# Performance work log

Measured on AMD Instinct MI355X. Metric: run time of the kernel, lower is better.

## Reference

```python
import jax, jax.numpy as jnp
import numpy as np

N = 6
DT = 0.02
EPS = 1e-6
_R, _C = np.tril_indices(N)  # row-major lower-triangle order, matches the torch double loop


def _mlp(x, W1, b1, W2, b2, W3, b3):
    h = jax.nn.softplus(x @ W1 + b1)
    h = jax.nn.softplus(h @ W2 + b2)
    return h @ W3 + b3


def _trig(q):
    # interleaved [cos q0, sin q0, cos q1, sin q1, ...]
    return jnp.stack([jnp.cos(q), jnp.sin(q)], axis=-1).reshape(q.shape[:-1] + (2 * N,))


def _mass_single(q, pL):
    # q: (6,) -> M: (6,6)
    y = _mlp(_trig(q), *pL)  # (21,)
    L = jnp.zeros((N, N), y.dtype).at[_R, _C].set(y)
    return L @ L.T + EPS * jnp.eye(N, dtype=y.dtype)


def _mass_batched(q, pL):
    y = _mlp(_trig(q), *pL)  # (B,21)
    L = jnp.zeros((q.shape[0], N, N), y.dtype).at[:, _R, _C].set(y)
    return jnp.einsum('bik,bjk->bij', L, L) + EPS * jnp.eye(N, dtype=y.dtype)


def _pot_batched(q, pV):
    return _mlp(_trig(q), *pV)[:, 0]  # (B,)


def _get_acc(q, qdot, a, pL, pV):
    M = _mass_batched(q, pL)                                   # (B,6,6)
    # per-sample Jacobian dM[i,j]/dq[k] -> (B,6,6,6)
    dM_dq = jax.vmap(jax.jacfwd(lambda qq: _mass_single(qq, pL)))(q)
    # torch: term_1[b,i,j,l] = sum_k M[b,l,k] * dM[b,j,k]/dq[b,i]
    term1 = jnp.einsum('blk,bjki->bijl', M, dM_dq)
    dM = term1 + term1.swapaxes(2, 3)
    c = (jnp.einsum('bjik,bk,bj->bi', dM, qdot, qdot)
         - 0.5 * jnp.einsum('bikj,bk,bj->bi', dM, qdot, qdot))
    # faithful to torch.cholesky_inverse(M): inverse of tril(M) @ tril(M)^T
    Linv = jnp.linalg.inv(jnp.tril(M))
    Minv = Linv.swapaxes(-1, -2) @ Linv
    dV_dq = jax.grad(lambda qq: _pot_batched(qq, pV).sum())(q)  # (B,6)
    return jnp.einsum('bij,bj->bi', Minv, a - c - dV_dq)


def _derivs(s, a, pL, pV):
    q, qdot = s[:, :N], s[:, N:]
    qddot = _get_acc(q, qdot, a, pL, pV)
    return jnp.concatenate([qdot, qddot], axis=1)


def _rk2(s, a, pL, pV):
    alpha = 2.0 / 3.0
    k1 = _derivs(s, a, pL, pV)
    k2 = _derivs(s + alpha * DT * k1, a, pL, pV)
    return s + DT * ((1.0 - 1.0 / (2.0 * alpha)) * k1 + (1.0 / (2.0 * alpha)) * k2)


def setup_inputs() -> dict:
    key = jax.random.key(0)
    ks = jax.random.split(key, 16)
    B = 32768
    def lin(kw, kb, fin, fout):
        s = 1.0 / np.sqrt(fin)
        return (jax.random.uniform(kw, (fin, fout), jnp.float32, -s, s),
                jax.random.uniform(kb, (fout,), jnp.float32, -s, s))
    W1L, b1L = lin(ks[0], ks[1], 12, 128)
    W2L, b2L = lin(ks[2], ks[3], 128, 128)
    W3L, b3L = lin(ks[4], ks[5], 128, 21)
    W1V, b1V = lin(ks[6], ks[7], 12, 128)
    W2V, b2V = lin(ks[8], ks[9], 128, 128)
    W3V, b3V = lin(ks[10], ks[11], 128, 1)
    o = jax.random.normal(ks[12], (B, 18), jnp.float32)
    a = jax.random.normal(ks[13], (B, 6), jnp.float32)
    return {"o": o, "a": a,
            "W1L": W1L, "b1L": b1L, "W2L": W2L, "b2L": b2L, "W3L": W3L, "b3L": b3L,
            "W1V": W1V, "b1V": b1V, "W2V": W2V, "b2V": b2V, "W3V": W3V, "b3V": b3V}


def reference(o, a, W1L, b1L, W2L, b2L, W3L, b3L, W1V, b1V, W2V, b2V, W3V, b3V):
    pL = (W1L, b1L, W2L, b2L, W3L, b3L)
    pV = (W1V, b1V, W2V, b2V, W3V, b3V)
    s = o[:, :2 * N]
    s_next = _rk2(s, a, pL, pV)
    return jnp.concatenate([s_next, o[:, 2 * N:]], axis=1)
```

## Files before the change

### kernel.cpp

```cpp
#include <hip/hip_runtime.h>

#define SMP 64
#define NW 8
#define NT (NW*64)

constexpr float DTc  = 0.02f;
constexpr float ADc  = (2.0f/3.0f)*0.02f;
constexpr float EPSc = 1e-6f;

#define FQ   0
#define FQD  6
#define FT   12
#define FL   24
#define FM   45
#define FDV  81
#define FC1  87
#define FC2  93
#define FKQ  99
#define FGT  105
#define SSTR 117

#define HS 129

__device__ __forceinline__ float softplusf(float z) {
    return fmaxf(z, 0.0f) + __logf(1.0f + __expf(-fabsf(z)));
}
__device__ __forceinline__ float sigmoidf_(float z) {
    float t = __expf(-fabsf(z));
    float r = 1.0f / (1.0f + t);
    return z >= 0.0f ? r : t * r;
}

__global__ void prep_kernel(const float* __restrict__ W1L, const float* __restrict__ W1V,
                            const float* __restrict__ W2V, float* __restrict__ ws) {
    int idx = blockIdx.x*256 + threadIdx.x;
    if (idx < 1536) {
        int n = idx / 12, d = idx % 12;
        ws[idx] = W1L[d*128 + n];
    } else if (idx < 3072) {
        int j = idx - 1536;
        int m = j / 12, d = j % 12;
        ws[idx] = W1V[d*128 + m];
    } else if (idx < 19456) {
        int j = idx - 3072;
        int n = j / 128, m = j % 128;
        ws[idx] = W2V[m*128 + n];
    }
}

__launch_bounds__(NT)
__global__ void lnn_kernel(
    const float* __restrict__ o,   const float* __restrict__ aIn,
    const float* __restrict__ b1L, const float* __restrict__ W2L,
    const float* __restrict__ b2L, const float* __restrict__ W3L,
    const float* __restrict__ b3L,
    const float* __restrict__ b1V, const float* __restrict__ W2V,
    const float* __restrict__ b2V, const float* __restrict__ W3V,
    const float* __restrict__ W1LT, const float* __restrict__ W1VT,
    const float* __restrict__ W2VT,
    float* __restrict__ out)
{
    __shared__ float H1[SMP*HS];
    __shared__ float H2[SMP*HS];
    __shared__ float GH[SMP*HS];
    __shared__ float S[SMP*SSTR];

    const int tid  = threadIdx.x;
    const int lane = tid & 63;
    const int wv   = __builtin_amdgcn_readfirstlane(tid >> 6);
    const int gs   = blockIdx.x * SMP + lane;
    float* Sl = &S[lane*SSTR];
    float* Hrow1 = &H1[lane*HS];
    float* Hrow2 = &H2[lane*HS];
    float* HrowG = &GH[lane*HS];

    constexpr int TRW[21] = {0,1,1,2,2,2,3,3,3,3,4,4,4,4,4,5,5,5,5,5,5};
    constexpr int TCW[21] = {0,0,1,0,1,2,0,1,2,3,0,1,2,3,4,0,1,2,3,4,5};

    for (int stage = 0; stage < 2; ++stage) {
        float qv[6];
        if (stage == 0) {
            #pragma unroll
            for (int i = 0; i < 6; ++i) qv[i] = o[gs*18+i];
            if (wv == 0) {
                #pragma unroll
                for (int i = 0; i < 6; ++i) { Sl[FQ+i] = qv[i]; Sl[FQD+i] = o[gs*18+6+i]; }
            }
        } else {
            #pragma unroll
            for (int i = 0; i < 6; ++i) qv[i] = Sl[FQ+i];
        }
        float tt[12];
        #pragma unroll
        for (int i = 0; i < 6; ++i) { tt[2*i] = cosf(qv[i]); tt[2*i+1] = sinf(qv[i]); }
        if (wv == 0) {
            #pragma unroll
            for (int d = 0; d < 12; ++d) Sl[FT+d] = tt[d];
        } else if (wv == 1) {
            #pragma unroll
            for (int k = 0; k < 21; ++k) Sl[FL+k] = b3L[k];
        } else if (wv == 2) {
            #pragma unroll
            for (int i = 0; i < 6; ++i) { Sl[FC1+i] = 0.0f; Sl[FC2+i] = 0.0f; }
        } else if (wv == 3) {
            #pragma unroll
            for (int d = 0; d < 12; ++d) Sl[FGT+d] = 0.0f;
        }
        {
            const int m0 = __builtin_amdgcn_readfirstlane(wv * 16);
            #pragma unroll
            for (int j = 0; j < 16; ++j) {
                int m = m0 + j;
                const float4* w4 = (const float4*)&W1VT[m*12];
                float4 wa = w4[0], wb = w4[1], wc = w4[2];
                float z = b1V[m];
                z += tt[0]*wa.x + tt[1]*wa.y + tt[2]*wa.z + tt[3]*wa.w;
                z += tt[4]*wb.x + tt[5]*wb.y + tt[6]*wb.z + tt[7]*wb.w;
                z += tt[8]*wc.x + tt[9]*wc.y + tt[10]*wc.z + tt[11]*wc.w;
                Hrow2[m] = softplusf(z);
            }
        }
        __syncthreads();

        {
            const int n0 = __builtin_amdgcn_readfirstlane(wv * 16);
            #pragma unroll
            for (int j = 0; j < 16; ++j) {
                int n = n0 + j;
                const float4* w4 = (const float4*)&W1LT[n*12];
                float4 wa = w4[0], wb = w4[1], wc = w4[2];
                float z = b1L[n];
                z += tt[0]*wa.x + tt[1]*wa.y + tt[2]*wa.z + tt[3]*wa.w;
                z += tt[4]*wb.x + tt[5]*wb.y + tt[6]*wb.z + tt[7]*wb.w;
                z += tt[8]*wc.x + tt[9]*wc.y + tt[10]*wc.z + tt[11]*wc.w;
                Hrow1[n] = softplusf(z);
            }
            float acc[16];
            #pragma unroll
            for (int j = 0; j < 16; ++j) acc[j] = b2V[n0+j];
            for (int m8 = 0; m8 < 128; m8 += 8) {
                float hr[8];
                #pragma unroll
                for (int t = 0; t < 8; ++t) hr[t] = Hrow2[m8+t];
                #pragma unroll
                for (int t = 0; t < 8; ++t) {
                    const float4* w4 = (const float4*)&W2V[(m8+t)*128 + n0];
                    #pragma unroll
                    for (int g = 0; g < 4; ++g) {
                        float4 w = w4[g];
                        acc[4*g+0] += hr[t]*w.x; acc[4*g+1] += hr[t]*w.y;
                        acc[4*g+2] += hr[t]*w.z; acc[4*g+3] += hr[t]*w.w;
                    }
                }
            }
            #pragma unroll
            for (int j = 0; j < 16; ++j) {
                int n = n0 + j;
                HrowG[n] = sigmoidf_(acc[j]) * W3V[n];
            }
        }
        __syncthreads();

        {
            const int n0 = __builtin_amdgcn_readfirstlane(wv * 16);
            float sig1v[16];
            #pragma unroll
            for (int i = 0; i < 16; ++i) sig1v[i] = 1.0f - __expf(-Hrow2[n0+i]);

            float acc[16];
            #pragma unroll
            for (int j = 0; j < 16; ++j) acc[j] = b2L[n0+j];
            for (int m8 = 0; m8 < 128; m8 += 8) {
                float hr[8];
                #pragma unroll
                for (int t = 0; t < 8; ++t) hr[t] = Hrow1[m8+t];
                #pragma unroll
                for (int t = 0; t < 8; ++t) {
                    const float4* w4 = (const float4*)&W2L[(m8+t)*128 + n0];
                    #pragma unroll
                    for (int g = 0; g < 4; ++g) {
                        float4 w = w4[g];
                        acc[4*g+0] += hr[t]*w.x; acc[4*g+1] += hr[t]*w.y;
                        acc[4*g+2] += hr[t]*w.z; acc[4*g+3] += hr[t]*w.w;
                    }
                }
            }
            float yp[21];
            #pragma unroll
            for (int k = 0; k < 21; ++k) yp[k] = 0.0f;
            #pragma unroll
            for (int j = 0; j < 16; ++j) {
                int n = n0 + j;
                float h2 = softplusf(acc[j]);
                Hrow2[n] = h2;
                #pragma unroll
                for (int k = 0; k < 21; ++k) yp[k] += h2 * W3L[n*21 + k];
            }
            #pragma unroll
            for (int k = 0; k < 21; ++k) atomicAdd(&Sl[FL+k], yp[k]);

            float ga[16];
            #pragma unroll
            for (int i = 0; i < 16; ++i) ga[i] = 0.0f;
            for (int n8 = 0; n8 < 128; n8 += 8) {
                float gr[8];
                #pragma unroll
                for (int t = 0; t < 8; ++t) gr[t] = HrowG[n8+t];
                #pragma unroll
                for (int t = 0; t < 8; ++t) {
                    const float4* w4 = (const float4*)&W2VT[(n8+t)*128 + n0];
                    #pragma unroll
                    for (int g = 0; g < 4; ++g) {
                        float4 w = w4[g];
                        ga[4*g+0] += gr[t]*w.x; ga[4*g+1] += gr[t]*w.y;
                        ga[4*g+2] += gr[t]*w.z; ga[4*g+3] += gr[t]*w.w;
                    }
                }
            }
            float gtp[12];
            #pragma unroll
            for (int d = 0; d < 12; ++d) gtp[d] = 0.0f;
            #pragma unroll
            for (int i = 0; i < 16; ++i) {
                int m = n0 + i;
                float g1h = ga[i] * sig1v[i];
                const float4* w4 = (const float4*)&W1VT[m*12];
                float4 wa = w4[0], wb = w4[1], wc = w4[2];
                gtp[0] += g1h*wa.x; gtp[1] += g1h*wa.y; gtp[2]  += g1h*wa.z; gtp[3]  += g1h*wa.w;
                gtp[4] += g1h*wb.x; gtp[5] += g1h*wb.y; gtp[6]  += g1h*wb.z; gtp[7]  += g1h*wb.w;
                gtp[8] += g1h*wc.x; gtp[9] += g1h*wc.y; gtp[10] += g1h*wc.z; gtp[11] += g1h*wc.w;
            }
            #pragma unroll
            for (int d = 0; d < 12; ++d) atomicAdd(&Sl[FGT+d], gtp[d]);
        }
        __syncthreads();

        if (wv < 6) {
            int i = wv;
            for (int j = 0; j < 6; ++j) {
                float s = 0.0f;
                int mn = (i < j) ? i : j;
                for (int k = 0; k <= mn; ++k)
                    s += Sl[FL + (i*(i+1))/2 + k] * Sl[FL + (j*(j+1))/2 + k];
                if (i == j) s += EPSc;
                Sl[FM + i*6 + j] = s;
            }
        } else if (wv == 6) {
            #pragma unroll
            for (int i = 0; i < 6; ++i)
                Sl[FDV+i] = -tt[2*i+1]*Sl[FGT+2*i] + tt[2*i]*Sl[FGT+2*i+1];
        }
        {
            const int n0 = __builtin_amdgcn_readfirstlane(wv * 16);
            float v1[16], v2[16];
            #pragma unroll
            for (int i = 0; i < 16; ++i) { v1[i] = Hrow1[n0+i]; v2[i] = Hrow2[n0+i]; }
            #pragma unroll
            for (int i = 0; i < 16; ++i) {
                Hrow1[n0+i] = 1.0f - __expf(-v1[i]);
                Hrow2[n0+i] = 1.0f - __expf(-v2[i]);
            }
        }
        __syncthreads();

        {
            float qd[6], u6[6], p6[6], r6[6];
            #pragma unroll
            for (int i = 0; i < 6; ++i) qd[i] = Sl[FQD+i];
            #pragma unroll
            for (int i = 0; i < 6; ++i) {
                float s = 0.0f;
                #pragma unroll
                for (int j = 0; j < 6; ++j) s += Sl[FM+i*6+j]*qd[j];
                u6[i] = s;
            }
            #pragma unroll
            for (int i = 0; i < 6; ++i) { p6[i] = 0.0f; r6[i] = 0.0f; }
            #pragma unroll
            for (int t = 0; t < 21; ++t) {
                float Lv = Sl[FL+t];
                p6[TCW[t]] += Lv * qd[TRW[t]];
                r6[TCW[t]] += Lv * u6[TRW[t]];
            }

            for (int uu = wv; uu < 24; uu += NW) {
                const int d     = __builtin_amdgcn_readfirstlane(uu >> 2);
                const int mbase = __builtin_amdgcn_readfirstlane(((uu >> 1) & 1) * 64);
                const int nbase = __builtin_amdgcn_readfirstlane((uu & 1) * 64);
                float tc = Sl[FT+2*d], ts = Sl[FT+2*d+1];
                float acc[64];
                #pragma unroll
                for (int n = 0; n < 64; ++n) acc[n] = 0.0f;
                for (int m8 = 0; m8 < 64; m8 += 8) {
                    float s1r[8];
                    #pragma unroll
                    for (int t = 0; t < 8; ++t) s1r[t] = Hrow1[mbase + m8 + t];
                    #pragma unroll
                    for (int t = 0; t < 8; ++t) {
                        int mm = mbase + m8 + t;
                        float u1 = tc*W1LT[mm*12 + 2*d+1] - ts*W1LT[mm*12 + 2*d];
                        float dm = s1r[t]*u1;
                        const float4* w4 = (const float4*)&W2L[mm*128 + nbase];
                        #pragma unroll
                        for (int g = 0; g < 16; ++g) {
                            float4 w = w4[g];
                            acc[4*g+0] += dm*w.x; acc[4*g+1] += dm*w.y;
                            acc[4*g+2] += dm*w.z; acc[4*g+3] += dm*w.w;
                        }
                    }
                }
                float dy[21];
                #pragma unroll
                for (int k = 0; k < 21; ++k) dy[k] = 0.0f;
                for (int n4 = 0; n4 < 64; n4 += 4) {
                    float s2r[4];
                    #pragma unroll
                    for (int t = 0; t < 4; ++t) s2r[t] = Hrow2[nbase + n4 + t];
                    #pragma unroll
                    for (int t = 0; t < 4; ++t) {
                        int nn = nbase + n4 + t;
                        float d2 = s2r[t] * acc[n4+t];
                        const float* wr = &W3L[nn*21];
                        #pragma unroll
                        for (int k = 0; k < 21; ++k) dy[k] += d2 * wr[k];
                    }
                }
                float a1[6],a2[6],a3[6],a4[6];
                #pragma unroll
                for (int i = 0; i < 6; ++i) { a1[i]=0.f; a2[i]=0.f; a3[i]=0.f; a4[i]=0.f; }
                #pragma unroll
                for (int t = 0; t < 21; ++t) {
                    float dv = dy[t];
                    a1[TRW[t]] += dv * p6[TCW[t]];
                    a2[TCW[t]] += dv * qd[TRW[t]];
                    a3[TRW[t]] += dv * r6[TCW[t]];
                    a4[TCW[t]] += dv * u6[TRW[t]];
                }
                float w6[6], v6[6];
                #pragma unroll
                for (int i = 0; i < 6; ++i) { w6[i] = a1[i]; v6[i] = a3[i]; }
                #pragma unroll
                for (int t = 0; t < 21; ++t) {
                    float Lv = Sl[FL+t];
                    w6[TRW[t]] += Lv * a2[TCW[t]];
                    v6[TRW[t]] += Lv * a4[TCW[t]];
                }
                float qdd = Sl[FQD + d];
                float uw = 0.0f;
                #pragma unroll
                for (int i = 0; i < 6; ++i) {
                    float mw = 0.0f;
                    #pragma unroll
                    for (int j = 0; j < 6; ++j) mw += Sl[FM+i*6+j]*w6[j];
                    atomicAdd(&Sl[FC1+i], qdd*(v6[i]+mw));
                    uw += u6[i]*w6[i];
                }
                atomicAdd(&Sl[FC2+d], 2.0f*uw);
            }
        }
        __syncthreads();

        if (wv == 0) {
            float rhs[6];
            #pragma unroll
            for (int i = 0; i < 6; ++i) {
                float c = Sl[FC1+i] - 0.5f*Sl[FC2+i];
                rhs[i] = aIn[gs*6+i] - c - Sl[FDV+i];
            }
            float Mm[36];
            #pragma unroll
            for (int i = 0; i < 36; ++i) Mm[i] = Sl[FM+i];
            float Li[21];
            #pragma unroll
            for (int j = 0; j < 6; ++j) {
                float x[6];
                x[j] = 1.0f / Mm[j*6+j];
                #pragma unroll
                for (int i2 = j+1; i2 < 6; ++i2) {
                    float s = 0.0f;
                    #pragma unroll
                    for (int k = j; k < i2; ++k) s += Mm[i2*6+k]*x[k];
                    x[i2] = -s / Mm[i2*6+i2];
                }
                #pragma unroll
                for (int i2 = j; i2 < 6; ++i2) Li[(i2*(i2+1))/2 + j] = x[i2];
            }
            float y1[6];
            #pragma unroll
            for (int i = 0; i < 6; ++i) {
                float s = 0.0f;
                #pragma unroll
                for (int j = 0; j <= i; ++j) s += Li[(i*(i+1))/2+j]*rhs[j];
                y1[i] = s;
            }
            float qdd2[6];
            #pragma unroll
            for (int i = 0; i < 6; ++i) {
                float s = 0.0f;
                #pragma unroll
                for (int k = i; k < 6; ++k) s += Li[(k*(k+1))/2+i]*y1[k];
                qdd2[i] = s;
            }
            if (stage == 0) {
                #pragma unroll
                for (int i = 0; i < 6; ++i) Sl[FKQ+i] = qdd2[i];
                #pragma unroll
                for (int i = 0; i < 6; ++i) Sl[FQ+i] += ADc*Sl[FQD+i];
                #pragma unroll
                for (int i = 0; i < 6; ++i) Sl[FQD+i] += ADc*qdd2[i];
            } else {
                #pragma unroll
                for (int i = 0; i < 6; ++i) {
                    float q0 = o[gs*18+i], qd0 = o[gs*18+6+i];
                    out[gs*18+i]    = q0  + DTc*(0.25f*qd0      + 0.75f*Sl[FQD+i]);
                    out[gs*18+6+i]  = qd0 + DTc*(0.25f*Sl[FKQ+i] + 0.75f*qdd2[i]);
                    out[gs*18+12+i] = o[gs*18+12+i];
                }
            }
        }
        __syncthreads();
    }
}

extern "C" void kernel_launch(void* const* d_in, const int* in_sizes, int n_in,
                              void* d_out, int out_size, void* d_ws, size_t ws_size,
                              hipStream_t stream) {
    const float* o   = (const float*)d_in[0];
    const float* a   = (const float*)d_in[1];
    const float* W1L = (const float*)d_in[2];
    const float* b1L = (const float*)d_in[3];
    const float* W2L = (const float*)d_in[4];
    const float* b2L = (const float*)d_in[5];
    const float* W3L = (const float*)d_in[6];
    const float* b3L = (const float*)d_in[7];
    const float* W1V = (const float*)d_in[8];
    const float* b1V = (const float*)d_in[9];
    const float* W2V = (const float*)d_in[10];
    const float* b2V = (const float*)d_in[11];
    const float* W3V = (const float*)d_in[12];
    float* ws   = (float*)d_ws;
    float* outp = (float*)d_out;

    hipLaunchKernelGGL(prep_kernel, dim3(76), dim3(256), 0, stream, W1L, W1V, W2V, ws);
    hipLaunchKernelGGL(lnn_kernel, dim3(32768/SMP), dim3(NT), 0, stream,
        o, a, b1L, W2L, b2L, W3L, b3L, b1V, W2V, b2V, W3V,
        ws, ws + 1536, ws + 3072, outp);
}
```

Before: 622.5 us.

## Reorganize mass-matrix Jacobian per wave to reuse W2L across all six q-derivatives

The Jacobian stage now gives each wave a fixed 16-column slice of the second layer and accumulates all six q-derivatives at once in a 96-entry accumulator. Each W2L and W1LT load is reused six times, and per-d shared-memory atomics are replaced by register accumulation followed by a single flush per wave. The layer-2 forward pass and the potential-gradient backward matmul are fused into one loop over m. Launch bounds now request two blocks per CU. The large accumulator plus the occupancy hint risks register spills.

```diff
diff --git a/kernel.cpp b/kernel.cpp
--- a/kernel.cpp
+++ b/kernel.cpp
@@ -48,7 +48,7 @@
     }
 }
 
-__launch_bounds__(NT)
+__launch_bounds__(NT, 2)
 __global__ void lnn_kernel(
     const float* __restrict__ o,   const float* __restrict__ aIn,
     const float* __restrict__ b1L, const float* __restrict__ W2L,
@@ -167,21 +167,25 @@
             #pragma unroll
             for (int i = 0; i < 16; ++i) sig1v[i] = 1.0f - __expf(-Hrow2[n0+i]);
 
-            float acc[16];
-            #pragma unroll
-            for (int j = 0; j < 16; ++j) acc[j] = b2L[n0+j];
+            float acc[16], ga[16];
+            #pragma unroll
+            for (int j = 0; j < 16; ++j) { acc[j] = b2L[n0+j]; ga[j] = 0.0f; }
             for (int m8 = 0; m8 < 128; m8 += 8) {
-                float hr[8];
-                #pragma unroll
-                for (int t = 0; t < 8; ++t) hr[t] = Hrow1[m8+t];
+                float hr[8], gr[8];
+                #pragma unroll
+                for (int t = 0; t < 8; ++t) { hr[t] = Hrow1[m8+t]; gr[t] = HrowG[m8+t]; }
                 #pragma unroll
                 for (int t = 0; t < 8; ++t) {
                     const float4* w4 = (const float4*)&W2L[(m8+t)*128 + n0];
+                    const float4* v4 = (const float4*)&W2VT[(m8+t)*128 + n0];
                     #pragma unroll
                     for (int g = 0; g < 4; ++g) {
                         float4 w = w4[g];
                         acc[4*g+0] += hr[t]*w.x; acc[4*g+1] += hr[t]*w.y;
                         acc[4*g+2] += hr[t]*w.z; acc[4*g+3] += hr[t]*w.w;
+                        float4 v = v4[g];
+                        ga[4*g+0] += gr[t]*v.x; ga[4*g+1] += gr[t]*v.y;
+                        ga[4*g+2] += gr[t]*v.z; ga[4*g+3] += gr[t]*v.w;
                     }
                 }
             }
@@ -199,24 +203,6 @@
             #pragma unroll
             for (int k = 0; k < 21; ++k) atomicAdd(&Sl[FL+k], yp[k]);
 
-            float ga[16];
-            #pragma unroll
-            for (int i = 0; i < 16; ++i) ga[i] = 0.0f;
-            for (int n8 = 0; n8 < 128; n8 += 8) {
-                float gr[8];
-                #pragma unroll
-                for (int t = 0; t < 8; ++t) gr[t] = HrowG[n8+t];
-                #pragma unroll
-                for (int t = 0; t < 8; ++t) {
-                    const float4* w4 = (const float4*)&W2VT[(n8+t)*128 + n0];
-                    #pragma unroll
-                    for (int g = 0; g < 4; ++g) {
-                        float4 w = w4[g];
-                        ga[4*g+0] += gr[t]*w.x; ga[4*g+1] += gr[t]*w.y;
-                        ga[4*g+2] += gr[t]*w.z; ga[4*g+3] += gr[t]*w.w;
-                    }
-                }
-            }
             float gtp[12];
             #pragma unroll
             for (int d = 0; d < 12; ++d) gtp[d] = 0.0f;
@@ -283,47 +269,62 @@
                 r6[TCW[t]] += Lv * u6[TRW[t]];
             }
 
-            for (int uu = wv; uu < 24; uu += NW) {
-                const int d     = __builtin_amdgcn_readfirstlane(uu >> 2);
-                const int mbase = __builtin_amdgcn_readfirstlane(((uu >> 1) & 1) * 64);
-                const int nbase = __builtin_amdgcn_readfirstlane((uu & 1) * 64);
-                float tc = Sl[FT+2*d], ts = Sl[FT+2*d+1];
-                float acc[64];
-                #pragma unroll
-                for (int n = 0; n < 64; ++n) acc[n] = 0.0f;
-                for (int m8 = 0; m8 < 64; m8 += 8) {
-                    float s1r[8];
-                    #pragma unroll
-                    for (int t = 0; t < 8; ++t) s1r[t] = Hrow1[mbase + m8 + t];
-                    #pragma unroll
-                    for (int t = 0; t < 8; ++t) {
-                        int mm = mbase + m8 + t;
-                        float u1 = tc*W1LT[mm*12 + 2*d+1] - ts*W1LT[mm*12 + 2*d];
-                        float dm = s1r[t]*u1;
-                        const float4* w4 = (const float4*)&W2L[mm*128 + nbase];
+            const int n0 = __builtin_amdgcn_readfirstlane(wv * 16);
+
+            float acc[96];
+            #pragma unroll
+            for (int i = 0; i < 96; ++i) acc[i] = 0.0f;
+
+            for (int m2 = 0; m2 < 128; m2 += 2) {
+                float s1a = Hrow1[m2];
+                float s1b = Hrow1[m2+1];
+                #pragma unroll
+                for (int half = 0; half < 2; ++half) {
+                    const int mm = m2 + half;
+                    const float s1 = half ? s1b : s1a;
+                    const float4* w1 = (const float4*)&W1LT[mm*12];
+                    float4 wa = w1[0], wb = w1[1], wc = w1[2];
+                    float dm[6];
+                    dm[0] = s1*(tt[0]*wa.y - tt[1]*wa.x);
+                    dm[1] = s1*(tt[2]*wa.w - tt[3]*wa.z);
+                    dm[2] = s1*(tt[4]*wb.y - tt[5]*wb.x);
+                    dm[3] = s1*(tt[6]*wb.w - tt[7]*wb.z);
+                    dm[4] = s1*(tt[8]*wc.y - tt[9]*wc.x);
+                    dm[5] = s1*(tt[10]*wc.w - tt[11]*wc.z);
+                    const float4* w2 = (const float4*)&W2L[mm*128 + n0];
+                    #pragma unroll
+                    for (int g = 0; g < 4; ++g) {
+                        float4 w = w2[g];
                         #pragma unroll
-                        for (int g = 0; g < 16; ++g) {
-                            float4 w = w4[g];
-                            acc[4*g+0] += dm*w.x; acc[4*g+1] += dm*w.y;
-                            acc[4*g+2] += dm*w.z; acc[4*g+3] += dm*w.w;
+                        for (int d = 0; d < 6; ++d) {
+                            acc[d*16 + 4*g+0] += dm[d]*w.x;
+                            acc[d*16 + 4*g+1] += dm[d]*w.y;
+                            acc[d*16 + 4*g+2] += dm[d]*w.z;
+                            acc[d*16 + 4*g+3] += dm[d]*w.w;
                         }
                     }
                 }
+            }
+
+            float sig2s[16];
+            #pragma unroll
+            for (int j = 0; j < 16; ++j) sig2s[j] = Hrow2[n0+j];
+
+            float c1loc[6], c2loc[6];
+            #pragma unroll
+            for (int i = 0; i < 6; ++i) { c1loc[i] = 0.0f; c2loc[i] = 0.0f; }
+
+            #pragma unroll
+            for (int d = 0; d < 6; ++d) {
                 float dy[21];
                 #pragma unroll
                 for (int k = 0; k < 21; ++k) dy[k] = 0.0f;
-                for (int n4 = 0; n4 < 64; n4 += 4) {
-                    float s2r[4];
-                    #pragma unroll
-                    for (int t = 0; t < 4; ++t) s2r[t] = Hrow2[nbase + n4 + t];
-                    #pragma unroll
-                    for (int t = 0; t < 4; ++t) {
-                        int nn = nbase + n4 + t;
-                        float d2 = s2r[t] * acc[n4+t];
-                        const float* wr = &W3L[nn*21];
-                        #pragma unroll
-                        for (int k = 0; k < 21; ++k) dy[k] += d2 * wr[k];
-                    }
+                #pragma unroll
+                for (int j = 0; j < 16; ++j) {
+                    float d2 = sig2s[j] * acc[d*16+j];
+                    const float* wr = &W3L[(n0+j)*21];
+                    #pragma unroll
+                    for (int k = 0; k < 21; ++k) dy[k] += d2 * wr[k];
                 }
                 float a1[6],a2[6],a3[6],a4[6];
                 #pragma unroll
@@ -345,18 +346,22 @@
                     w6[TRW[t]] += Lv * a2[TCW[t]];
                     v6[TRW[t]] += Lv * a4[TCW[t]];
                 }
-                float qdd = Sl[FQD + d];
+                float qdd = qd[d];
                 float uw = 0.0f;
                 #pragma unroll
                 for (int i = 0; i < 6; ++i) {
                     float mw = 0.0f;
                     #pragma unroll
                     for (int j = 0; j < 6; ++j) mw += Sl[FM+i*6+j]*w6[j];
-                    atomicAdd(&Sl[FC1+i], qdd*(v6[i]+mw));
+                    c1loc[i] += qdd*(v6[i]+mw);
                     uw += u6[i]*w6[i];
                 }
-                atomicAdd(&Sl[FC2+d], 2.0f*uw);
-            }
+                c2loc[d] = 2.0f*uw;
+            }
+            #pragma unroll
+            for (int i = 0; i < 6; ++i) atomicAdd(&Sl[FC1+i], c1loc[i]);
+            #pragma unroll
+            for (int d = 0; d < 6; ++d) atomicAdd(&Sl[FC2+d], c2loc[d]);
         }
         __syncthreads();
 
```

New measurement: 577.0 us. 1.08x faster.
